# Optimization experiments

Hardware: AMD Instinct MI355X
Metric: run time of the kernel (lower is better)

Reference implementation:

```python
import jax, jax.numpy as jnp
import numpy as np

STRIDE = 2
PAD = 1
K = 4
OUT_PAD = 0


def setup_inputs() -> dict:
    key = jax.random.key(0)
    k1, k2, k3, k4 = jax.random.split(key, 4)
    x = jax.random.normal(k1, (16, 64, 128, 128), dtype=jnp.float32)
    # torch ConvTranspose2d weight layout: [in_channels, out_channels, kH, kW]
    w = jax.random.normal(k2, (64, 32, 4, 4), dtype=jnp.float32) * 0.05
    conv_b = jax.random.normal(k3, (32,), dtype=jnp.float32) * 0.05
    bias = jax.random.normal(k4, (1, 1, 1, 1), dtype=jnp.float32)
    return {"x": x, "w": w, "conv_b": conv_b, "bias": bias}


def conv_transpose2d(x, w, conv_b):
    # Equivalent of torch ConvTranspose2d(k=4, s=2, p=1, op=0):
    # dilate input by stride, pad by k-1-p (+op on trailing side), conv with flipped kernel.
    lo = K - 1 - PAD
    hi = K - 1 - PAD + OUT_PAD
    w_oihw = jnp.flip(w, axis=(2, 3)).transpose(1, 0, 2, 3)  # [Cout, Cin, kH, kW]
    y = jax.lax.conv_general_dilated(
        x, w_oihw,
        window_strides=(1, 1),
        padding=((lo, hi), (lo, hi)),
        lhs_dilation=(STRIDE, STRIDE),
        dimension_numbers=("NCHW", "OIHW", "NCHW"),
    )
    return y + conv_b[None, :, None, None]


def reference(x, w, conv_b, bias):
    y = conv_transpose2d(x, w, conv_b)          # [N, Cout, H', W']
    y = jnp.min(y, axis=1, keepdims=True)       # channel-min -> [N,1,H',W']
    y = jnp.sum(y, axis=2, keepdims=True)       # height-sum  -> [N,1,1,W']
    # kernel uses tanh-based GELU approximation
    return jax.nn.gelu(y, approximate=True) + bias
```

## Files before the change

kernel.cpp:

```cpp
#include <hip/hip_runtime.h>
#include <math.h>

typedef __attribute__((ext_vector_type(8))) short short8;
typedef __attribute__((ext_vector_type(16))) float f32x16;
typedef __attribute__((ext_vector_type(2))) unsigned uintx2;

#define XS_STRIDE 72
#define NROWS 6

__device__ __forceinline__ short f2bf(float f) {
    union { float f; unsigned u; } v; v.f = f;
    unsigned r = (v.u + 0x7FFFu + ((v.u >> 16) & 1u)) >> 16;
    return (short)r;
}

__device__ __forceinline__ unsigned cvt_pk_bf16(float lo, float hi) {
    unsigned r;
    asm("v_cvt_pk_bf16_f32 %0, %1, %2" : "=v"(r) : "v"(lo), "v"(hi));
    return r;
}

__device__ __forceinline__ void bar_lds() {
    asm volatile("s_waitcnt lgkmcnt(0)" ::: "memory");
    __builtin_amdgcn_s_barrier();
}

__global__ void prep(const float* __restrict__ w, short* __restrict__ wfrag,
                     float* __restrict__ acc, unsigned* __restrict__ ctr) {
    if (blockIdx.x >= 128) {
        #pragma unroll
        for (int i = 0; i < 16; ++i) acc[i * 256 + threadIdx.x] = 0.f;
        if (threadIdx.x < 16) ctr[threadIdx.x] = 0u;
        return;
    }
    int idx = blockIdx.x * 256 + threadIdx.x;
    int j    = idx & 7;
    int lane = (idx >> 3) & 63;
    int q    = (idx >> 9) & 15;
    int p    = idx >> 13;
    int co = lane & 31, hf = lane >> 5;
    int ci = (q & 3) * 16 + hf * 8 + j;
    int tq = q >> 2, a = tq >> 1, b = tq & 1;
    int ph = p >> 1, pw = p & 1;
    int kh = 2 * a + 1 - ph, kw = 2 * b + 1 - pw;
    wfrag[idx] = f2bf(w[((ci * 32 + co) * 4 + kh) * 4 + kw]);
}

__global__ __launch_bounds__(256, 3) void convt_mfma(
    const float* __restrict__ x, const short* __restrict__ wfrag,
    const float* __restrict__ conv_b, float* __restrict__ acc,
    unsigned* __restrict__ ctr, const float* __restrict__ bias,
    float* __restrict__ out)
{
    __shared__ short xs[NROWS][34][XS_STRIDE];
    __shared__ float minbuf[4][32];
    __shared__ unsigned lastf;

    int blk = ((blockIdx.x & 7) << 8) | (blockIdx.x >> 3);
    const int jq = blk & 3, st = (blk >> 2) & 31, n = blk >> 7;
    const int t  = threadIdx.x;
    const int i0 = st * 4;

    const int wv = t >> 6, lane = t & 63;
    const int ph = wv >> 1, pw = wv & 1;
    const int ln = lane & 31, half = lane >> 5;

    const float* xn = x + (size_t)n * 64 * 128 * 128;
    const int col  = t & 31;
    const int cib  = (t >> 5) * 8;
    const int gcol = jq * 32 + col;

    float pfA[8], pfB[8];
    auto load_row = [&](int r, float* dst) {
        int gi = i0 - 1 + r;
        bool rowok = (unsigned)gi < 128u;
        int gic = rowok ? gi : 0;
        const float* px = xn + ((size_t)cib * 128 + gic) * 128 + gcol;
        #pragma unroll
        for (int c = 0; c < 8; ++c) dst[c] = rowok ? px[c * 16384] : 0.f;
    };
    auto write_row = [&](int r, const float* src) {
        uintx2 u0, u1;
        u0.x = cvt_pk_bf16(src[0], src[1]); u0.y = cvt_pk_bf16(src[2], src[3]);
        u1.x = cvt_pk_bf16(src[4], src[5]); u1.y = cvt_pk_bf16(src[6], src[7]);
        *(uintx2*)&xs[r][col + 1][cib]     = u0;
        *(uintx2*)&xs[r][col + 1][cib + 4] = u1;
    };
    load_row(0, pfA);
    load_row(1, pfB);
    write_row(0, pfA); load_row(2, pfA);
    write_row(1, pfB); load_row(3, pfB);
    write_row(2, pfA); load_row(4, pfA);
    write_row(3, pfB); load_row(5, pfB);
    write_row(4, pfA);
    write_row(5, pfB);

    float hv[3];
    #pragma unroll
    for (int q = 0; q < 3; ++q) {
        int idx = q * 256 + t;
        int r = idx >> 7, side = (idx >> 6) & 1, ci = idx & 63;
        int gi = i0 - 1 + r;
        int gc = jq * 32 + (side ? 32 : -1);
        hv[q] = ((unsigned)gi < 128u && (unsigned)gc < 128u)
              ? xn[((size_t)ci * 128 + gi) * 128 + gc] : 0.f;
    }
    #pragma unroll
    for (int q = 0; q < 3; ++q) {
        int idx = q * 256 + t;
        int r = idx >> 7, side = (idx >> 6) & 1, ci = idx & 63;
        xs[r][side ? 33 : 0][ci] = f2bf(hv[q]);
    }

    short8 af[16];
    {
        const short8* wf = (const short8*)(wfrag + wv * 8192);
        #pragma unroll
        for (int q = 0; q < 16; ++q) af[q] = wf[q * 64 + lane];
    }
    float cb[16];
    #pragma unroll
    for (int reg = 0; reg < 16; ++reg)
        cb[reg] = conv_b[(reg & 3) + 8 * (reg >> 2) + 4 * half];

    bar_lds();

    float osum = 0.f;
    #pragma unroll
    for (int k = 0; k < 2; ++k) {
        const int L0 = 2 * k + ph;
        f32x16 acc0, acc1;
        #pragma unroll
        for (int reg = 0; reg < 16; ++reg) { acc0[reg] = cb[reg]; acc1[reg] = cb[reg]; }
        __builtin_amdgcn_s_setprio(1);
        #pragma unroll
        for (int b = 0; b < 2; ++b) {
            int colp = ln + (pw - b) + 1;
            const short* p0 = &xs[L0][colp][half * 8];
            const short* p1 = &xs[L0 + 1][colp][half * 8];
            const short* p2 = &xs[L0 + 2][colp][half * 8];
            #pragma unroll
            for (int c = 0; c < 4; ++c) {
                short8 Fs = *(const short8*)(p1 + c * 16);
                acc0 = __builtin_amdgcn_mfma_f32_32x32x16_bf16(af[4*b+c],   Fs, acc0, 0, 0, 0);
                acc1 = __builtin_amdgcn_mfma_f32_32x32x16_bf16(af[8+4*b+c], Fs, acc1, 0, 0, 0);
                short8 F0 = *(const short8*)(p0 + c * 16);
                acc0 = __builtin_amdgcn_mfma_f32_32x32x16_bf16(af[8+4*b+c], F0, acc0, 0, 0, 0);
                short8 F2 = *(const short8*)(p2 + c * 16);
                acc1 = __builtin_amdgcn_mfma_f32_32x32x16_bf16(af[4*b+c],   F2, acc1, 0, 0, 0);
            }
        }
        __builtin_amdgcn_s_setprio(0);

        float mn0, mn1;
        {
            float a = fminf(fminf(acc0[0], acc0[1]), fminf(acc0[2], acc0[3]));
            float b2 = fminf(fminf(acc0[4], acc0[5]), fminf(acc0[6], acc0[7]));
            float c = fminf(fminf(acc0[8], acc0[9]), fminf(acc0[10], acc0[11]));
            float d = fminf(fminf(acc0[12], acc0[13]), fminf(acc0[14], acc0[15]));
            mn0 = fminf(fminf(a, b2), fminf(c, d));
            a = fminf(fminf(acc1[0], acc1[1]), fminf(acc1[2], acc1[3]));
            b2 = fminf(fminf(acc1[4], acc1[5]), fminf(acc1[6], acc1[7]));
            c = fminf(fminf(acc1[8], acc1[9]), fminf(acc1[10], acc1[11]));
            d = fminf(fminf(acc1[12], acc1[13]), fminf(acc1[14], acc1[15]));
            mn1 = fminf(fminf(a, b2), fminf(c, d));
        }
        mn0 = fminf(mn0, __shfl_xor(mn0, 32, 64));
        mn1 = fminf(mn1, __shfl_xor(mn1, 32, 64));
        osum += mn0 + mn1;
    }

    if (half == 0) minbuf[wv][ln] = osum;
    bar_lds();

    if (t < 64) {
        int c = t & 31, pwp = t >> 5;
        float v = minbuf[pwp][c] + minbuf[2 + pwp][c];
        int ow = ((jq * 32 + c) << 1) | pwp;
        atomicAdd(&acc[n * 256 + ow], v);
    }
    __syncthreads();
    if (t == 0) lastf = (atomicAdd(&ctr[n], 1u) == 127u) ? 1u : 0u;
    __syncthreads();

    if (lastf) {
        __threadfence();
        float s = __hip_atomic_load(&acc[n * 256 + t], __ATOMIC_RELAXED,
                                    __HIP_MEMORY_SCOPE_AGENT);
        float u = 0.7978845608028654f * (s + 0.044715f * s * s * s);
        out[n * 256 + t] = 0.5f * s * (1.f + tanhf(u)) + bias[0];
    }
}

extern "C" void kernel_launch(void* const* d_in, const int* in_sizes, int n_in,
                              void* d_out, int out_size, void* d_ws, size_t ws_size,
                              hipStream_t stream) {
    const float* x      = (const float*)d_in[0];
    const float* w      = (const float*)d_in[1];
    const float* conv_b = (const float*)d_in[2];
    const float* bias   = (const float*)d_in[3];
    float* out = (float*)d_out;

    short*    wfrag = (short*)d_ws;
    float*    acc   = (float*)((char*)d_ws + 65536);
    unsigned* ctr   = (unsigned*)((char*)d_ws + 65536 + 16384);

    hipLaunchKernelGGL(prep, dim3(129), dim3(256), 0, stream, w, wfrag, acc, ctr);
    hipLaunchKernelGGL(convt_mfma, dim3(16 * 32 * 4), dim3(256), 0, stream,
                       x, wfrag, conv_b, acc, ctr, bias, out);
}
```

Before: 119.5 us.

## Double column tile per block to amortize weight fragment loads and halo

Each block now covers 64 input columns instead of 32, which halves the grid to 1024 blocks. Every wave runs two column sub-tiles, so its 16 weight fragment registers, conv-bias setup and halo loads are shared across twice the work. LDS staging grows to 66 columns, and the global-to-LDS writes become 16-byte stores of 16 channels. The cost is more LDS and registers per block, with launch bounds lowered to 2 blocks per CU, and fewer blocks in flight to hide global load latency.

```diff
diff --git a/kernel.cpp b/kernel.cpp
--- a/kernel.cpp
+++ b/kernel.cpp
@@ -3,7 +3,7 @@
 
 typedef __attribute__((ext_vector_type(8))) short short8;
 typedef __attribute__((ext_vector_type(16))) float f32x16;
-typedef __attribute__((ext_vector_type(2))) unsigned uintx2;
+typedef __attribute__((ext_vector_type(4))) unsigned uintx4;
 
 #define XS_STRIDE 72
 #define NROWS 6
@@ -46,18 +46,18 @@
     wfrag[idx] = f2bf(w[((ci * 32 + co) * 4 + kh) * 4 + kw]);
 }
 
-__global__ __launch_bounds__(256, 3) void convt_mfma(
+__global__ __launch_bounds__(256, 2) void convt_mfma(
     const float* __restrict__ x, const short* __restrict__ wfrag,
     const float* __restrict__ conv_b, float* __restrict__ acc,
     unsigned* __restrict__ ctr, const float* __restrict__ bias,
     float* __restrict__ out)
 {
-    __shared__ short xs[NROWS][34][XS_STRIDE];
-    __shared__ float minbuf[4][32];
+    __shared__ short xs[NROWS][66][XS_STRIDE];
+    __shared__ float minbuf[4][64];
     __shared__ unsigned lastf;
 
-    int blk = ((blockIdx.x & 7) << 8) | (blockIdx.x >> 3);
-    const int jq = blk & 3, st = (blk >> 2) & 31, n = blk >> 7;
+    int blk = ((blockIdx.x & 7) << 7) | (blockIdx.x >> 3);
+    const int jh = blk & 1, st = (blk >> 1) & 31, n = blk >> 6;
     const int t  = threadIdx.x;
     const int i0 = st * 4;
 
@@ -66,25 +66,27 @@
     const int ln = lane & 31, half = lane >> 5;
 
     const float* xn = x + (size_t)n * 64 * 128 * 128;
-    const int col  = t & 31;
-    const int cib  = (t >> 5) * 8;
-    const int gcol = jq * 32 + col;
-
-    float pfA[8], pfB[8];
+    const int col  = t & 63;
+    const int cib  = (t >> 6) * 16;
+    const int gcol = jh * 64 + col;
+
+    float pfA[16], pfB[16];
     auto load_row = [&](int r, float* dst) {
         int gi = i0 - 1 + r;
         bool rowok = (unsigned)gi < 128u;
         int gic = rowok ? gi : 0;
         const float* px = xn + ((size_t)cib * 128 + gic) * 128 + gcol;
         #pragma unroll
-        for (int c = 0; c < 8; ++c) dst[c] = rowok ? px[c * 16384] : 0.f;
+        for (int c = 0; c < 16; ++c) dst[c] = rowok ? px[c * 16384] : 0.f;
     };
     auto write_row = [&](int r, const float* src) {
-        uintx2 u0, u1;
-        u0.x = cvt_pk_bf16(src[0], src[1]); u0.y = cvt_pk_bf16(src[2], src[3]);
-        u1.x = cvt_pk_bf16(src[4], src[5]); u1.y = cvt_pk_bf16(src[6], src[7]);
-        *(uintx2*)&xs[r][col + 1][cib]     = u0;
-        *(uintx2*)&xs[r][col + 1][cib + 4] = u1;
+        uintx4 u0, u1;
+        u0.x = cvt_pk_bf16(src[0], src[1]);   u0.y = cvt_pk_bf16(src[2], src[3]);
+        u0.z = cvt_pk_bf16(src[4], src[5]);   u0.w = cvt_pk_bf16(src[6], src[7]);
+        u1.x = cvt_pk_bf16(src[8], src[9]);   u1.y = cvt_pk_bf16(src[10], src[11]);
+        u1.z = cvt_pk_bf16(src[12], src[13]); u1.w = cvt_pk_bf16(src[14], src[15]);
+        *(uintx4*)&xs[r][col + 1][cib]     = u0;
+        *(uintx4*)&xs[r][col + 1][cib + 8] = u1;
     };
     load_row(0, pfA);
     load_row(1, pfB);
@@ -101,7 +103,7 @@
         int idx = q * 256 + t;
         int r = idx >> 7, side = (idx >> 6) & 1, ci = idx & 63;
         int gi = i0 - 1 + r;
-        int gc = jq * 32 + (side ? 32 : -1);
+        int gc = jh * 64 + (side ? 64 : -1);
         hv[q] = ((unsigned)gi < 128u && (unsigned)gc < 128u)
               ? xn[((size_t)ci * 128 + gi) * 128 + gc] : 0.f;
     }
@@ -109,7 +111,7 @@
     for (int q = 0; q < 3; ++q) {
         int idx = q * 256 + t;
         int r = idx >> 7, side = (idx >> 6) & 1, ci = idx & 63;
-        xs[r][side ? 33 : 0][ci] = f2bf(hv[q]);
+        xs[r][side ? 65 : 0][ci] = f2bf(hv[q]);
     }
 
     short8 af[16];
@@ -125,62 +127,66 @@
 
     bar_lds();
 
-    float osum = 0.f;
+    float osum0 = 0.f, osum1 = 0.f;
     #pragma unroll
     for (int k = 0; k < 2; ++k) {
         const int L0 = 2 * k + ph;
-        f32x16 acc0, acc1;
-        #pragma unroll
-        for (int reg = 0; reg < 16; ++reg) { acc0[reg] = cb[reg]; acc1[reg] = cb[reg]; }
-        __builtin_amdgcn_s_setprio(1);
-        #pragma unroll
-        for (int b = 0; b < 2; ++b) {
-            int colp = ln + (pw - b) + 1;
-            const short* p0 = &xs[L0][colp][half * 8];
-            const short* p1 = &xs[L0 + 1][colp][half * 8];
-            const short* p2 = &xs[L0 + 2][colp][half * 8];
+        #pragma unroll
+        for (int jb = 0; jb < 2; ++jb) {
+            f32x16 acc0, acc1;
             #pragma unroll
-            for (int c = 0; c < 4; ++c) {
-                short8 Fs = *(const short8*)(p1 + c * 16);
-                acc0 = __builtin_amdgcn_mfma_f32_32x32x16_bf16(af[4*b+c],   Fs, acc0, 0, 0, 0);
-                acc1 = __builtin_amdgcn_mfma_f32_32x32x16_bf16(af[8+4*b+c], Fs, acc1, 0, 0, 0);
-                short8 F0 = *(const short8*)(p0 + c * 16);
-                acc0 = __builtin_amdgcn_mfma_f32_32x32x16_bf16(af[8+4*b+c], F0, acc0, 0, 0, 0);
-                short8 F2 = *(const short8*)(p2 + c * 16);
-                acc1 = __builtin_amdgcn_mfma_f32_32x32x16_bf16(af[4*b+c],   F2, acc1, 0, 0, 0);
+            for (int reg = 0; reg < 16; ++reg) { acc0[reg] = cb[reg]; acc1[reg] = cb[reg]; }
+            __builtin_amdgcn_s_setprio(1);
+            #pragma unroll
+            for (int b = 0; b < 2; ++b) {
+                int colp = jb * 32 + ln + (pw - b) + 1;
+                const short* p0 = &xs[L0][colp][half * 8];
+                const short* p1 = &xs[L0 + 1][colp][half * 8];
+                const short* p2 = &xs[L0 + 2][colp][half * 8];
+                #pragma unroll
+                for (int c = 0; c < 4; ++c) {
+                    short8 Fs = *(const short8*)(p1 + c * 16);
+                    acc0 = __builtin_amdgcn_mfma_f32_32x32x16_bf16(af[4*b+c],   Fs, acc0, 0, 0, 0);
+                    acc1 = __builtin_amdgcn_mfma_f32_32x32x16_bf16(af[8+4*b+c], Fs, acc1, 0, 0, 0);
+                    short8 F0 = *(const short8*)(p0 + c * 16);
+                    acc0 = __builtin_amdgcn_mfma_f32_32x32x16_bf16(af[8+4*b+c], F0, acc0, 0, 0, 0);
+                    short8 F2 = *(const short8*)(p2 + c * 16);
+                    acc1 = __builtin_amdgcn_mfma_f32_32x32x16_bf16(af[4*b+c],   F2, acc1, 0, 0, 0);
+                }
             }
+            __builtin_amdgcn_s_setprio(0);
+
+            float mn0, mn1;
+            {
+                float a = fminf(fminf(acc0[0], acc0[1]), fminf(acc0[2], acc0[3]));
+                float b2 = fminf(fminf(acc0[4], acc0[5]), fminf(acc0[6], acc0[7]));
+                float c = fminf(fminf(acc0[8], acc0[9]), fminf(acc0[10], acc0[11]));
+                float d = fminf(fminf(acc0[12], acc0[13]), fminf(acc0[14], acc0[15]));
+                mn0 = fminf(fminf(a, b2), fminf(c, d));
+                a = fminf(fminf(acc1[0], acc1[1]), fminf(acc1[2], acc1[3]));
+                b2 = fminf(fminf(acc1[4], acc1[5]), fminf(acc1[6], acc1[7]));
+                c = fminf(fminf(acc1[8], acc1[9]), fminf(acc1[10], acc1[11]));
+                d = fminf(fminf(acc1[12], acc1[13]), fminf(acc1[14], acc1[15]));
+                mn1 = fminf(fminf(a, b2), fminf(c, d));
+            }
+            mn0 = fminf(mn0, __shfl_xor(mn0, 32, 64));
+            mn1 = fminf(mn1, __shfl_xor(mn1, 32, 64));
+            if (jb == 0) osum0 += mn0 + mn1;
+            else         osum1 += mn0 + mn1;
         }
-        __builtin_amdgcn_s_setprio(0);
-
-        float mn0, mn1;
-        {
-            float a = fminf(fminf(acc0[0], acc0[1]), fminf(acc0[2], acc0[3]));
-            float b2 = fminf(fminf(acc0[4], acc0[5]), fminf(acc0[6], acc0[7]));
-            float c = fminf(fminf(acc0[8], acc0[9]), fminf(acc0[10], acc0[11]));
-            float d = fminf(fminf(acc0[12], acc0[13]), fminf(acc0[14], acc0[15]));
-            mn0 = fminf(fminf(a, b2), fminf(c, d));
-            a = fminf(fminf(acc1[0], acc1[1]), fminf(acc1[2], acc1[3]));
-            b2 = fminf(fminf(acc1[4], acc1[5]), fminf(acc1[6], acc1[7]));
-            c = fminf(fminf(acc1[8], acc1[9]), fminf(acc1[10], acc1[11]));
-            d = fminf(fminf(acc1[12], acc1[13]), fminf(acc1[14], acc1[15]));
-            mn1 = fminf(fminf(a, b2), fminf(c, d));
-        }
-        mn0 = fminf(mn0, __shfl_xor(mn0, 32, 64));
-        mn1 = fminf(mn1, __shfl_xor(mn1, 32, 64));
-        osum += mn0 + mn1;
-    }
-
-    if (half == 0) minbuf[wv][ln] = osum;
+    }
+
+    if (half == 0) { minbuf[wv][ln] = osum0; minbuf[wv][32 + ln] = osum1; }
     bar_lds();
 
-    if (t < 64) {
-        int c = t & 31, pwp = t >> 5;
+    if (t < 128) {
+        int c = t & 63, pwp = (t >> 6) & 1;
         float v = minbuf[pwp][c] + minbuf[2 + pwp][c];
-        int ow = ((jq * 32 + c) << 1) | pwp;
+        int ow = ((jh * 64 + c) << 1) | pwp;
         atomicAdd(&acc[n * 256 + ow], v);
     }
     __syncthreads();
-    if (t == 0) lastf = (atomicAdd(&ctr[n], 1u) == 127u) ? 1u : 0u;
+    if (t == 0) lastf = (atomicAdd(&ctr[n], 1u) == 63u) ? 1u : 0u;
     __syncthreads();
 
     if (lastf) {
@@ -206,6 +212,6 @@
     unsigned* ctr   = (unsigned*)((char*)d_ws + 65536 + 16384);
 
     hipLaunchKernelGGL(prep, dim3(129), dim3(256), 0, stream, w, wfrag, acc, ctr);
-    hipLaunchKernelGGL(convt_mfma, dim3(16 * 32 * 4), dim3(256), 0, stream,
+    hipLaunchKernelGGL(convt_mfma, dim3(16 * 32 * 2), dim3(256), 0, stream,
                        x, wfrag, conv_b, acc, ctr, bias, out);
 }
```

New measurement: 115.1 us. -3.7%, faster.
